# Performance work log

Hardware: AMD Instinct MI355X
Metric: run time of the kernel (lower is better)

The kernel has to match this reference:

```python
import jax, jax.numpy as jnp
import numpy as np

N_HEADS = 16

def setup_inputs() -> dict:
    key = jax.random.key(0)
    k1, k2, k3 = jax.random.split(key, 3)
    d = 1024
    x = jax.random.normal(k1, (2, 2048, d), dtype=jnp.float32)
    W_in = jax.random.normal(k2, (d, 3 * d), dtype=jnp.float32) * (d ** -0.5)
    W_out = jax.random.normal(k3, (d, d), dtype=jnp.float32) * (d ** -0.5)
    return {"x": x, "W_in": W_in, "W_out": W_out}

def reference(x, W_in, W_out):
    B, S, D = x.shape
    H = N_HEADS
    Dh = D // H
    qkv = x @ W_in                                  # [B,S,3D]
    q, k, v = jnp.split(qkv, 3, axis=-1)
    # [B,S,D] -> [B,H,S,Dh]
    q = q.reshape(B, S, H, Dh).transpose(0, 2, 1, 3)
    k = k.reshape(B, S, H, Dh).transpose(0, 2, 1, 3)
    v = v.reshape(B, S, H, Dh).transpose(0, 2, 1, 3)
    scores = jnp.einsum('bhqd,bhkd->bhqk', q, k)    # [B,H,S,S]
    causal = jnp.triu(jnp.ones((S, S), dtype=bool), k=1)
    scores = jnp.where(causal, -jnp.inf, scores)
    scores = scores / jnp.sqrt(jnp.asarray(Dh, scores.dtype))
    attn = jax.nn.softmax(scores, axis=-1)
    out = jnp.einsum('bhqk,bhkd->bhqd', attn, v)    # [B,H,S,Dh]
    out = out.transpose(0, 2, 1, 3).reshape(B, S, D)
    return out @ W_out
```

## Files before the change

kernel.cpp:

```cpp
#include <hip/hip_runtime.h>
#include <cstdint>
#include <cstddef>

typedef __bf16 bf16;
typedef bf16  bf16x4  __attribute__((ext_vector_type(4)));
typedef bf16  bf16x8  __attribute__((ext_vector_type(8)));
typedef float floatx4 __attribute__((ext_vector_type(4)));

#define BATCH 2
#define SEQ   2048
#define DIM   1024
#define NH    16
#define DH    64
#define D3    3072
#define MROWS 4096

__device__ __forceinline__ void gld16(void* lds, const void* gptr) {
  __builtin_amdgcn_global_load_lds(
      (const __attribute__((address_space(1))) unsigned int*)gptr,
      (__attribute__((address_space(3))) unsigned int*)lds, 16, 0, 0);
}

__global__ __launch_bounds__(256) void k_prep(const float4* __restrict__ x,
                                              bf16* __restrict__ xb,
                                              const float* __restrict__ Wi,
                                              bf16* __restrict__ wti,
                                              const float* __restrict__ Wo,
                                              bf16* __restrict__ wto) {
  __shared__ float tile[32][33];
  const int bid = blockIdx.x;
  if (bid < 4096) {
    int i = bid * 256 + threadIdx.x;
    float4 v = x[i];
    bf16x4 o;
    o.x = (bf16)v.x; o.y = (bf16)v.y; o.z = (bf16)v.z; o.w = (bf16)v.w;
    *(bf16x4*)(xb + (size_t)i * 4) = o;
    return;
  }
  const float* W; bf16* Wt; int N, id;
  if (bid < 7168) { W = Wi; Wt = wti; N = 3072; id = bid - 4096; }
  else            { W = Wo; Wt = wto; N = 1024; id = bid - 7168; }
  const int nb = N / 32;
  int n0 = (id % nb) * 32, k0 = (id / nb) * 32;
  int tx = threadIdx.x & 31, ty = threadIdx.x >> 5;
#pragma unroll
  for (int i = 0; i < 4; i++)
    tile[ty + i * 8][tx] = W[(size_t)(k0 + ty + i * 8) * N + n0 + tx];
  __syncthreads();
#pragma unroll
  for (int i = 0; i < 4; i++)
    Wt[(size_t)(n0 + ty + i * 8) * 1024 + k0 + tx] = (bf16)tile[tx][ty + i * 8];
}

template <typename OutT, int MODE>
__global__ __launch_bounds__(256) void k_gemm_bt(const bf16* __restrict__ A,
                                                 const bf16* __restrict__ Bt,
                                                 OutT* __restrict__ C,
                                                 bf16* __restrict__ qk,
                                                 bf16* __restrict__ vt,
                                                 int M, int N, int K) {
  __shared__ __align__(16) bf16 As[2][128 * 32];
  __shared__ __align__(16) bf16 Bs[2][128 * 32];
  const int t = threadIdx.x, l = t & 63, w = t >> 6;
  const int wr = w >> 1, wc = w & 1;
  const int q = l >> 4, mm = l & 15;
  const int m0 = blockIdx.y * 128, n0 = blockIdx.x * 128;
  const int sw = (mm >> 1) & 3;

  auto stage = [&](int kt) {
    const int bp = kt & 1;
#pragma unroll
    for (int i = 0; i < 2; i++) {
      int c = t + i * 256;
      int row = c >> 2, pos = c & 3;
      int g = pos ^ ((row >> 1) & 3);
      gld16((char*)As[bp] + (size_t)c * 16, A  + (size_t)(m0 + row) * K + kt * 32 + g * 8);
      gld16((char*)Bs[bp] + (size_t)c * 16, Bt + (size_t)(n0 + row) * K + kt * 32 + g * 8);
    }
  };

  floatx4 acc[4][4] = {};
  const int nk = K >> 5;

  stage(0);
  __syncthreads();

  for (int kt = 0; kt < nk; kt++) {
    if (kt + 1 < nk) stage(kt + 1);
    const bf16* Ab = As[kt & 1];
    const bf16* Bb = Bs[kt & 1];
    bf16x8 af[4], bfr[4];
#pragma unroll
    for (int mt = 0; mt < 4; mt++)
      af[mt] = *(const bf16x8*)(Ab + (size_t)(wr * 64 + mt * 16 + mm) * 32 + (q ^ sw) * 8);
#pragma unroll
    for (int nt = 0; nt < 4; nt++)
      bfr[nt] = *(const bf16x8*)(Bb + (size_t)(wc * 64 + nt * 16 + mm) * 32 + (q ^ sw) * 8);
#pragma unroll
    for (int mt = 0; mt < 4; mt++)
#pragma unroll
      for (int nt = 0; nt < 4; nt++)
        acc[mt][nt] = __builtin_amdgcn_mfma_f32_16x16x32_bf16(af[mt], bfr[nt],
                                                              acc[mt][nt], 0, 0, 0);
    if (kt + 1 < nk) __syncthreads();
  }
#pragma unroll
  for (int mt = 0; mt < 4; mt++)
#pragma unroll
    for (int nt = 0; nt < 4; nt++)
#pragma unroll
      for (int r = 0; r < 4; r++) {
        int row = m0 + wr * 64 + mt * 16 + q * 4 + r;
        int col = n0 + wc * 64 + nt * 16 + mm;
        if (MODE == 0) {
          C[(size_t)row * N + col] = (OutT)acc[mt][nt][r];
        } else {
          if (n0 < 2048) {
            qk[(size_t)row * 2048 + col] = (bf16)acc[mt][nt][r];
          } else {
            int d = col - 2048;
            int hh = d >> 6, dh = d & 63;
            int bb = row >> 11, s = row & 2047;
            vt[((size_t)(bb * 16 + hh) * 64 + dh) * SEQ + s] = (bf16)acc[mt][nt][r];
          }
        }
      }
}

__global__ __launch_bounds__(256, 4) void k_attn(const bf16* __restrict__ qk,
                                                 const bf16* __restrict__ vt,
                                                 bf16* __restrict__ out) {
  const int bx = blockIdx.x;
  const int qt = 31 - (bx >> 5);
  const int bh = bx & 31;
  const int b = bh >> 4, h = bh & 15;
  const int t = threadIdx.x, l = t & 63, w = t >> 6;
  const int q4 = l >> 4, mm = l & 15;
  const int sw = (mm >> 1) & 3;

  __shared__ __align__(16) char lds[8192 + 16384 + 16384];
  bf16* Qs = (bf16*)lds;
  bf16* Ps = (bf16*)lds;
  bf16* Ks = (bf16*)(lds + 8192);
  bf16* Vs = (bf16*)(lds + 8192 + 16384);

  const size_t qkbase = (size_t)b * SEQ * 2048;
  const size_t vtbase = (size_t)bh * 64 * SEQ;

  auto stage = [&](int kt) {
    const int bp = kt & 1;
#pragma unroll
    for (int i = 0; i < 2; i++) {
      int row = t >> 2, pos = t & 3;
      int g = pos ^ ((row >> 1) & 3);
      gld16((char*)(Ks + bp * 4096) + ((size_t)t + i * 256) * 16,
            qk + qkbase + (size_t)(kt * 64 + row) * 2048 + 1024 + h * 64 + i * 32 + g * 8);
    }
#pragma unroll
    for (int i = 0; i < 2; i++) {
      int c = t + i * 256;
      int vr = c >> 3, vc = c & 7;
      int src = vc ^ (vr & 7);
      gld16((char*)(Vs + bp * 4096) + (size_t)c * 16,
            vt + vtbase + (size_t)vr * SEQ + kt * 64 + src * 8);
    }
  };

  {
    int row = t >> 2, col = (t & 3) * 8;
#pragma unroll
    for (int i = 0; i < 2; i++)
      gld16((char*)Qs + ((size_t)t + i * 256) * 16,
            qk + qkbase + (size_t)(qt * 64 + row) * 2048 + h * 64 + i * 32 + col);
  }
  stage(0);
  __syncthreads();
  bf16x8 qf[2];
#pragma unroll
  for (int ks = 0; ks < 2; ks++) {
    qf[ks] = *(const bf16x8*)(Qs + (size_t)(ks * 64 + w * 16 + mm) * 32 + q4 * 8);
#pragma unroll
    for (int j = 0; j < 8; j++)
      qf[ks][j] = (bf16)((float)qf[ks][j] * 0.18033688f);
  }
  __syncthreads();

  float l_i = 0.f;
  floatx4 oaccT[4] = {};
  const int qloc = w * 16 + mm;
  const float FM = 24.0f;

  bf16* Pw = Ps + (size_t)w * 640;

  for (int kt = 0; kt <= qt; kt++) {
    if (kt < qt) stage(kt + 1);
    const bf16* Kb = Ks + (kt & 1) * 4096;
    const bf16* Vb = Vs + (kt & 1) * 4096;

    floatx4 sacc[4] = {};
#pragma unroll
    for (int ks = 0; ks < 2; ks++)
#pragma unroll
      for (int ct = 0; ct < 4; ct++) {
        bf16x8 kf = *(const bf16x8*)(Kb + (size_t)(ks * 64 + ct * 16 + mm) * 32 + (q4 ^ sw) * 8);
        sacc[ct] = __builtin_amdgcn_mfma_f32_16x16x32_bf16(kf, qf[ks], sacc[ct], 0, 0, 0);
      }

    bf16x4 pk[4];
    float rsum = 0.f;
    if (kt == qt) {
#pragma unroll
      for (int ct = 0; ct < 4; ct++)
#pragma unroll
        for (int r = 0; r < 4; r++) {
          float e = (ct * 16 + q4 * 4 + r > qloc)
                        ? 0.f : __builtin_amdgcn_exp2f(sacc[ct][r] - FM);
          pk[ct][r] = (bf16)e;
          rsum += e;
        }
    } else {
#pragma unroll
      for (int ct = 0; ct < 4; ct++)
#pragma unroll
        for (int r = 0; r < 4; r++) {
          float e = __builtin_amdgcn_exp2f(sacc[ct][r] - FM);
          pk[ct][r] = (bf16)e;
          rsum += e;
        }
    }
    rsum += __shfl_xor(rsum, 16, 64);
    rsum += __shfl_xor(rsum, 32, 64);
    l_i += rsum;

#pragma unroll
    for (int ks = 0; ks < 2; ks++) {
      *(bf16x4*)(Pw + (size_t)mm * 40 + q4 * 4)      = pk[ks * 2 + 0];
      *(bf16x4*)(Pw + (size_t)mm * 40 + 16 + q4 * 4) = pk[ks * 2 + 1];
      bf16x8 pf = *(const bf16x8*)(Pw + (size_t)mm * 40 + q4 * 8);
#pragma unroll
      for (int nt = 0; nt < 4; nt++) {
        int chunk = (ks * 4 + q4) ^ (mm & 7);
        bf16x8 vf = *(const bf16x8*)(Vb + (size_t)(nt * 16 + mm) * 64 + chunk * 8);
        oaccT[nt] = __builtin_amdgcn_mfma_f32_16x16x32_bf16(vf, pf, oaccT[nt], 0, 0, 0);
      }
    }

    if (kt < qt) __syncthreads();
  }

  float inv = 1.0f / l_i;
  int qrow = qt * 64 + qloc;
  bf16* orow = out + ((size_t)b * SEQ + qrow) * DIM + h * 64;
#pragma unroll
  for (int nt = 0; nt < 4; nt++) {
    bf16x4 o4;
#pragma unroll
    for (int r = 0; r < 4; r++) o4[r] = (bf16)(oaccT[nt][r] * inv);
    *(bf16x4*)(orow + nt * 16 + q4 * 4) = o4;
  }
}

extern "C" void kernel_launch(void* const* d_in, const int* in_sizes, int n_in,
                              void* d_out, int out_size, void* d_ws, size_t ws_size,
                              hipStream_t stream) {
  const float* x     = (const float*)d_in[0];
  const float* W_in  = (const float*)d_in[1];
  const float* W_out = (const float*)d_in[2];
  float* out = (float*)d_out;

  char* ws = (char*)d_ws;
  bf16* xb   = (bf16*)(ws);
  bf16* wti  = (bf16*)(ws + 8388608);
  bf16* wto  = (bf16*)(ws + 14680064);
  bf16* qkb  = (bf16*)(ws + 16777216);
  bf16* vtb  = (bf16*)(ws + 33554432);
  bf16* attn = xb;

  k_prep<<<8192, 256, 0, stream>>>((const float4*)x, xb, W_in, wti, W_out, wto);
  k_gemm_bt<bf16, 1><<<dim3(24, 32), 256, 0, stream>>>(xb, wti, nullptr, qkb, vtb,
                                                       MROWS, D3, DIM);
  k_attn<<<1024, 256, 0, stream>>>(qkb, vtb, attn);
  k_gemm_bt<float, 0><<<dim3(8, 32), 256, 0, stream>>>(attn, wto, out, nullptr, nullptr,
                                                       MROWS, DIM, DIM);
}
```

Baseline: 180.8 us.

## Remap GEMM blocks per XCD and use narrower tiles for output projection

Flattens the GEMM grid to 1D and remaps block indices so that blocks landing on the same XCD share A row tiles and neighbouring B column tiles, which should improve L2 reuse. The output projection switches to 128x64 tiles with four warps stacked along M, doubling its block count to better fill the CUs. The narrower tile lowers the MFMA-to-load ratio per block in exchange for more parallelism.

```diff
diff --git a/kernel.cpp b/kernel.cpp
--- a/kernel.cpp
+++ b/kernel.cpp
@@ -52,7 +52,7 @@
     Wt[(size_t)(n0 + ty + i * 8) * 1024 + k0 + tx] = (bf16)tile[tx][ty + i * 8];
 }
 
-template <typename OutT, int MODE>
+template <typename OutT, int MODE, int BN, int NPX>
 __global__ __launch_bounds__(256) void k_gemm_bt(const bf16* __restrict__ A,
                                                  const bf16* __restrict__ Bt,
                                                  OutT* __restrict__ C,
@@ -60,11 +60,15 @@
                                                  bf16* __restrict__ vt,
                                                  int M, int N, int K) {
   __shared__ __align__(16) bf16 As[2][128 * 32];
-  __shared__ __align__(16) bf16 Bs[2][128 * 32];
+  __shared__ __align__(16) bf16 Bs[2][BN * 32];
   const int t = threadIdx.x, l = t & 63, w = t >> 6;
-  const int wr = w >> 1, wc = w & 1;
   const int q = l >> 4, mm = l & 15;
-  const int m0 = blockIdx.y * 128, n0 = blockIdx.x * 128;
+  const int x = blockIdx.x & 7, g = blockIdx.x >> 3;
+  const int m0 = (g / NPX) * 128;
+  const int n0 = (x * NPX + g % NPX) * BN;
+  constexpr int MT = (BN == 128) ? 4 : 2;
+  const int mo = (BN == 128) ? ((w >> 1) * 64) : (w * 32);
+  const int no = (BN == 128) ? ((w & 1) * 64) : 0;
   const int sw = (mm >> 1) & 3;
 
   auto stage = [&](int kt) {
@@ -73,13 +77,19 @@
     for (int i = 0; i < 2; i++) {
       int c = t + i * 256;
       int row = c >> 2, pos = c & 3;
-      int g = pos ^ ((row >> 1) & 3);
-      gld16((char*)As[bp] + (size_t)c * 16, A  + (size_t)(m0 + row) * K + kt * 32 + g * 8);
-      gld16((char*)Bs[bp] + (size_t)c * 16, Bt + (size_t)(n0 + row) * K + kt * 32 + g * 8);
+      int gs = pos ^ ((row >> 1) & 3);
+      gld16((char*)As[bp] + (size_t)c * 16, A + (size_t)(m0 + row) * K + kt * 32 + gs * 8);
+    }
+#pragma unroll
+    for (int i = 0; i < BN / 64; i++) {
+      int c = t + i * 256;
+      int row = c >> 2, pos = c & 3;
+      int gs = pos ^ ((row >> 1) & 3);
+      gld16((char*)Bs[bp] + (size_t)c * 16, Bt + (size_t)(n0 + row) * K + kt * 32 + gs * 8);
     }
   };
 
-  floatx4 acc[4][4] = {};
+  floatx4 acc[MT][4] = {};
   const int nk = K >> 5;
 
   stage(0);
@@ -89,15 +99,15 @@
     if (kt + 1 < nk) stage(kt + 1);
     const bf16* Ab = As[kt & 1];
     const bf16* Bb = Bs[kt & 1];
-    bf16x8 af[4], bfr[4];
-#pragma unroll
-    for (int mt = 0; mt < 4; mt++)
-      af[mt] = *(const bf16x8*)(Ab + (size_t)(wr * 64 + mt * 16 + mm) * 32 + (q ^ sw) * 8);
+    bf16x8 af[MT], bfr[4];
+#pragma unroll
+    for (int mt = 0; mt < MT; mt++)
+      af[mt] = *(const bf16x8*)(Ab + (size_t)(mo + mt * 16 + mm) * 32 + (q ^ sw) * 8);
 #pragma unroll
     for (int nt = 0; nt < 4; nt++)
-      bfr[nt] = *(const bf16x8*)(Bb + (size_t)(wc * 64 + nt * 16 + mm) * 32 + (q ^ sw) * 8);
-#pragma unroll
-    for (int mt = 0; mt < 4; mt++)
+      bfr[nt] = *(const bf16x8*)(Bb + (size_t)(no + nt * 16 + mm) * 32 + (q ^ sw) * 8);
+#pragma unroll
+    for (int mt = 0; mt < MT; mt++)
 #pragma unroll
       for (int nt = 0; nt < 4; nt++)
         acc[mt][nt] = __builtin_amdgcn_mfma_f32_16x16x32_bf16(af[mt], bfr[nt],
@@ -105,17 +115,17 @@
     if (kt + 1 < nk) __syncthreads();
   }
 #pragma unroll
-  for (int mt = 0; mt < 4; mt++)
+  for (int mt = 0; mt < MT; mt++)
 #pragma unroll
     for (int nt = 0; nt < 4; nt++)
 #pragma unroll
       for (int r = 0; r < 4; r++) {
-        int row = m0 + wr * 64 + mt * 16 + q * 4 + r;
-        int col = n0 + wc * 64 + nt * 16 + mm;
+        int row = m0 + mo + mt * 16 + q * 4 + r;
+        int col = n0 + no + nt * 16 + mm;
         if (MODE == 0) {
           C[(size_t)row * N + col] = (OutT)acc[mt][nt][r];
         } else {
-          if (n0 < 2048) {
+          if (col < 2048) {
             qk[(size_t)row * 2048 + col] = (bf16)acc[mt][nt][r];
           } else {
             int d = col - 2048;
@@ -277,9 +287,9 @@
   bf16* attn = xb;
 
   k_prep<<<8192, 256, 0, stream>>>((const float4*)x, xb, W_in, wti, W_out, wto);
-  k_gemm_bt<bf16, 1><<<dim3(24, 32), 256, 0, stream>>>(xb, wti, nullptr, qkb, vtb,
-                                                       MROWS, D3, DIM);
+  k_gemm_bt<bf16, 1, 128, 3><<<768, 256, 0, stream>>>(xb, wti, nullptr, qkb, vtb,
+                                                      MROWS, D3, DIM);
   k_attn<<<1024, 256, 0, stream>>>(qkb, vtb, attn);
-  k_gemm_bt<float, 0><<<dim3(8, 32), 256, 0, stream>>>(attn, wto, out, nullptr, nullptr,
-                                                       MROWS, DIM, DIM);
-}
+  k_gemm_bt<float, 0, 64, 2><<<512, 256, 0, stream>>>(attn, wto, out, nullptr, nullptr,
+                                                      MROWS, DIM, DIM);
+}
```

New measurement: 183.5 us. No clear change (+1.5%).
